# Kernel tuning notes

Hardware: AMD Instinct MI355X
Metric: run time of the kernel (lower is better)

## Reference

```python
import jax, jax.numpy as jnp
import numpy as np

N_NODES = 50000
N_EDGES = 800000
N_FEAT = 64
N_HID = 64
N_CLASSES = 10
N_GRAPHS = 64


def setup_inputs() -> dict:
    key = jax.random.key(0)
    ks = jax.random.split(key, 14)
    # edge_index with no self-loops (PyG add_remaining_self_loops then appends
    # exactly one self loop per node, which the reference reproduces)
    row = jax.random.randint(ks[0], (N_EDGES,), 0, N_NODES, dtype=jnp.int32)
    off = jax.random.randint(ks[1], (N_EDGES,), 1, N_NODES, dtype=jnp.int32)
    col = (row + off) % N_NODES
    edge_index = jnp.stack([row, col])
    batch = jnp.sort(jax.random.randint(ks[2], (N_NODES,), 0, N_GRAPHS, dtype=jnp.int32))
    x = jax.random.normal(ks[3], (N_NODES, N_FEAT), jnp.float32)
    P_vec = jax.random.normal(ks[4], (N_EDGES,), jnp.float32)

    def lin(k, fi, fo):
        return jax.random.normal(k, (fi, fo), jnp.float32) * (1.0 / np.sqrt(fi))

    return {
        "x": x, "edge_index": edge_index, "batch": batch, "P_vec": P_vec,
        "W1": lin(ks[5], N_FEAT, N_HID), "b1": jax.random.normal(ks[6], (N_HID,)) * 0.02,
        "W2": lin(ks[7], N_HID, N_HID), "b2": jax.random.normal(ks[8], (N_HID,)) * 0.02,
        "W3": lin(ks[9], N_HID, N_HID), "b3": jax.random.normal(ks[10], (N_HID,)) * 0.02,
        "Wl": lin(ks[11], N_HID, N_CLASSES), "bl": jax.random.normal(ks[12], (N_CLASSES,)) * 0.02,
    }


def reference(x, edge_index, batch, P_vec, W1, b1, W2, b2, W3, b3, Wl, bl):
    n = x.shape[0]
    row, col = edge_index[0], edge_index[1]
    # add_remaining_self_loops: append one self loop per node with weight 1.0
    sl = jnp.arange(n, dtype=row.dtype)
    fr = jnp.concatenate([row, sl])          # [E+N] source
    fc = jnp.concatenate([col, sl])          # [E+N] target (flow source_to_target)
    w = jnp.concatenate([jax.nn.sigmoid(P_vec), jnp.ones((n,), x.dtype)])
    deg = jax.ops.segment_sum(w, fc, num_segments=n)
    dis = jnp.where(deg > 0, deg ** -0.5, 0.0)  # deg_inv_sqrt, inf->0
    norm = dis[fr] * w * dis[fc]             # identical for all 3 conv layers

    def gcn_layer(h, W, b):
        h = h @ W                             # Linear (no bias inside lin)
        agg = jax.ops.segment_sum(norm[:, None] * h[fr], fc, num_segments=n)
        return agg + b

    h = jax.nn.relu(gcn_layer(x, W1, b1))
    h = jax.nn.relu(gcn_layer(h, W2, b2))
    h = gcn_layer(h, W3, b3)
    # global_mean_pool over batch segment ids
    sums = jax.ops.segment_sum(h, batch, num_segments=N_GRAPHS)
    cnt = jax.ops.segment_sum(jnp.ones((n, 1), h.dtype), batch, num_segments=N_GRAPHS)
    pooled = sums / jnp.maximum(cnt, 1.0)
    # dropout is identity at inference; final classifier
    return pooled @ Wl + bl
```

## Files before the change

### kernel.cpp

```cpp
#include <hip/hip_runtime.h>
#include <hip/hip_bf16.h>
#include <hip/hip_fp16.h>
#include <math.h>

#define N_GRAPHS 64
#define N_CLASSES 10
#define FIXSCALE 262144.0f
#define MAXDEG 64

typedef __hip_bfloat16 bf16;
typedef int          i32x4 __attribute__((ext_vector_type(4)));
typedef _Float16     f16x8 __attribute__((ext_vector_type(8)));
typedef float        f32x4 __attribute__((ext_vector_type(4)));

__device__ __forceinline__ unsigned int pack_edge(int r, float s) {
    return ((unsigned int)r << 16) | (unsigned int)__half_as_ushort(__float2half(s));
}

__global__ void init_k(unsigned int* __restrict__ packed,
                       float* __restrict__ sums, float* __restrict__ cntG, int n) {
    int i = blockIdx.x * 256 + threadIdx.x;
    if (i < n) packed[i] = 0u;
    if (i < N_GRAPHS * 64) sums[i] = 0.0f;
    if (i < N_GRAPHS) cntG[i] = 0.0f;
}

__device__ __forceinline__ int bucket_of(int c) {
    int b = (int)(((unsigned int)c * 41u) >> 18);
    return b > 7 ? 7 : b;
}

__device__ __forceinline__ void do_edge(int c, int e, int myb,
                                        const int* __restrict__ row,
                                        const float* __restrict__ P,
                                        unsigned int* __restrict__ packed,
                                        unsigned int* __restrict__ ell) {
    if (bucket_of(c) == myb) {
        float s = 1.0f / (1.0f + expf(-P[e]));
        unsigned int rec = pack_edge(row[e], s);
        unsigned int fix = (unsigned int)(s * FIXSCALE + 0.5f);
        unsigned int old = atomicAdd(&packed[c], (1u << 24) | fix);
        unsigned int rank = old >> 24;
        if (rank < MAXDEG) ell[c * MAXDEG + rank] = rec;
    }
}

__global__ __launch_bounds__(256) void hist_k(const float* __restrict__ P,
                                              const int* __restrict__ row,
                                              const int* __restrict__ col,
                                              unsigned int* __restrict__ packed,
                                              unsigned int* __restrict__ ell, int E) {
    const int myb = blockIdx.x & 7;
    const int slice = blockIdx.x >> 3;
    const int E4 = E >> 2;
    const i32x4* col4 = (const i32x4*)col;
#pragma unroll
    for (int k = 0; k < 4; ++k) {
        int i4 = slice * 1024 + k * 256 + (int)threadIdx.x;
        if (i4 < E4) {
            i32x4 c = col4[i4];
            int e = i4 * 4;
            do_edge(c[0], e + 0, myb, row, P, packed, ell);
            do_edge(c[1], e + 1, myb, row, P, packed, ell);
            do_edge(c[2], e + 2, myb, row, P, packed, ell);
            do_edge(c[3], e + 3, myb, row, P, packed, ell);
        }
    }
    if (slice == 0) {
        for (int e = E4 * 4 + (int)threadIdx.x; e < E; e += 256)
            do_edge(col[e], e, myb, row, P, packed, ell);
    }
}

__global__ void disxg_k(const unsigned int* __restrict__ packed,
                        const float* __restrict__ x,
                        float* __restrict__ dis, bf16* __restrict__ xg,
                        unsigned int* __restrict__ ell, int n) {
    int i = blockIdx.x * 256 + threadIdx.x;
    if (i < n * 64) {
        int node = i >> 6;
        int lane = i & 63;
        unsigned int pk = packed[node];
        float deg = 1.0f + (float)(pk & 0xFFFFFFu) * (1.0f / FIXSCALE);
        float dv = 1.0f / sqrtf(deg);
        xg[i] = __float2bfloat16(x[i] * dv);
        if (lane == 0) dis[node] = dv;
        int cnt = (int)(pk >> 24);
        if (cnt > MAXDEG) cnt = MAXDEG;
        int pad = ((cnt + 7) & ~7) - cnt;
        if (lane < pad) ell[node * MAXDEG + cnt + lane] = 0u;
    }
}

__global__ void fold_k(const float* __restrict__ W3, const float* __restrict__ b3,
                       const float* __restrict__ Wl, const float* __restrict__ bl,
                       const float* __restrict__ W1, const float* __restrict__ W2,
                       float* __restrict__ Wc, float* __restrict__ bc,
                       __half* __restrict__ W1h, __half* __restrict__ W2h) {
    int t = blockIdx.x * 256 + threadIdx.x;
    if (t < 64 * N_CLASSES) {
        int k = t / N_CLASSES, c = t % N_CLASSES;
        float acc = 0.0f;
        for (int m = 0; m < 64; ++m) acc += W3[k * 64 + m] * Wl[m * N_CLASSES + c];
        Wc[t] = acc;
    }
    if (t < N_CLASSES) {
        float acc = bl[t];
        for (int m = 0; m < 64; ++m) acc += b3[m] * Wl[m * N_CLASSES + t];
        bc[t] = acc;
    }
    if (t < 8192) {
        int u = t & 4095;
        int j = u & 7, lane = (u >> 3) & 63, k2 = (u >> 9) & 1, tt = u >> 10;
        int srow = k2 * 32 + (lane >> 4) * 8 + j;
        int scol = tt * 16 + (lane & 15);
        const float* W = (t < 4096) ? W1 : W2;
        __half* Wh = (t < 4096) ? W1h : W2h;
        Wh[u] = __float2half(W[srow * 64 + scol]);
    }
}

__device__ __forceinline__ float edge_term(unsigned int v, const bf16* g, int lane) {
    int r = (int)(v >> 16);
    float s = __half2float(__ushort_as_half((unsigned short)(v & 0xFFFFu)));
    return s * __bfloat162float(g[r * 64 + lane]);
}

template <int OUTF>
__global__ __launch_bounds__(256) void agg_k(const bf16* __restrict__ g,
                                             const unsigned int* __restrict__ ell,
                                             const unsigned int* __restrict__ packed,
                                             const float* __restrict__ dis,
                                             float* __restrict__ out,
                                             __half* __restrict__ outH, int n) {
    int tid = threadIdx.x;
    int node = __builtin_amdgcn_readfirstlane(blockIdx.x * 4 + (tid >> 6));
    if (node >= n) return;
    int lane = tid & 63;

    float d = dis[node];
    int cnt = (int)(packed[node] >> 24);
    if (cnt > MAXDEG) cnt = MAXDEG;
    int cnt8 = (cnt + 7) & ~7;
    float acc = __bfloat162float(g[node * 64 + lane]);
    const unsigned int* rowp = ell + node * MAXDEG;

    float a[8];
#pragma unroll
    for (int t = 0; t < 8; ++t) a[t] = 0.0f;
    for (int j = 0; j < cnt8; j += 8) {
        unsigned int v[8];
#pragma unroll
        for (int t = 0; t < 8; ++t) v[t] = rowp[j + t];
#pragma unroll
        for (int t = 0; t < 8; ++t) a[t] += edge_term(v[t], g, lane);
    }
#pragma unroll
    for (int off = 4; off >= 1; off >>= 1)
#pragma unroll
        for (int t = 0; t < off; ++t) a[t] += a[t + off];
    acc += a[0];
    acc *= d;

    if (OUTF == 1) outH[(size_t)node * 64 + lane] = __float2half(acc);
    else           out[(size_t)node * 64 + lane] = acc;
}

__global__ __launch_bounds__(256) void gemm_k(const __half* __restrict__ A,
                                              const __half* __restrict__ Wsw,
                                              const float* __restrict__ b,
                                              const float* __restrict__ dis,
                                              bf16* __restrict__ outg, int n) {
    int tid = threadIdx.x;
    int grp = blockIdx.x * 4 + (tid >> 6);
    int rbase = grp * 16;
    if (rbase >= n) return;
    int l = tid & 63, lr = l & 15, lh = l >> 4;

    const f16x8* Ap = (const f16x8*)(A + (size_t)(rbase + lr) * 64 + lh * 8);
    f16x8 a0 = Ap[0];
    f16x8 a1 = Ap[4];
    const f16x8* Wp = (const f16x8*)Wsw;

    float dv[4];
#pragma unroll
    for (int r = 0; r < 4; ++r) dv[r] = dis[rbase + lh * 4 + r];

#pragma unroll
    for (int t = 0; t < 4; ++t) {
        f32x4 acc = {0.0f, 0.0f, 0.0f, 0.0f};
        acc = __builtin_amdgcn_mfma_f32_16x16x32_f16(a0, Wp[(t * 2 + 0) * 64 + l], acc, 0, 0, 0);
        acc = __builtin_amdgcn_mfma_f32_16x16x32_f16(a1, Wp[(t * 2 + 1) * 64 + l], acc, 0, 0, 0);
        int col = t * 16 + lr;
        float bc_ = b[col];
#pragma unroll
        for (int r = 0; r < 4; ++r) {
            float v = fmaxf(acc[r] + bc_, 0.0f) * dv[r];
            outg[(size_t)(rbase + lh * 4 + r) * 64 + col] = __float2bfloat16(v);
        }
    }
}

__global__ __launch_bounds__(256) void poolpart_k(const float* __restrict__ h,
                                                  const int* __restrict__ batch,
                                                  float* __restrict__ sums,
                                                  float* __restrict__ cntG, int n) {
    int wave = threadIdx.x >> 6, lane = threadIdx.x & 63;
    int base = blockIdx.x * 128 + wave * 32;
    if (base >= n) return;
    int end = base + 32; if (end > n) end = n;
    int g = batch[base];
    float acc = 0.0f;
    int run = 0;
    for (int i = base; i < end; ++i) {
        int gi = batch[i];
        if (gi != g) {
            atomicAdd(&sums[g * 64 + lane], acc);
            if (lane == 0) atomicAdd(&cntG[g], (float)run);
            g = gi; acc = 0.0f; run = 0;
        }
        acc += h[i * 64 + lane];
        ++run;
    }
    atomicAdd(&sums[g * 64 + lane], acc);
    if (lane == 0) atomicAdd(&cntG[g], (float)run);
}

__global__ void classify_k(const float* __restrict__ sums, const float* __restrict__ cntG,
                           const float* __restrict__ Wc, const float* __restrict__ bc,
                           float* __restrict__ out) {
    __shared__ float pooled[64];
    int g = blockIdx.x;
    int t = threadIdx.x;
    float inv = 1.0f / fmaxf(cntG[g], 1.0f);
    pooled[t] = sums[g * 64 + t] * inv;
    __syncthreads();
    if (t < N_CLASSES) {
        float acc = bc[t];
        for (int k = 0; k < 64; ++k) acc += pooled[k] * Wc[k * N_CLASSES + t];
        out[g * N_CLASSES + t] = acc;
    }
}

extern "C" void kernel_launch(void* const* d_in, const int* in_sizes, int n_in,
                              void* d_out, int out_size, void* d_ws, size_t ws_size,
                              hipStream_t stream) {
    const float* x     = (const float*)d_in[0];
    const int*   eidx  = (const int*)d_in[1];
    const int*   batch = (const int*)d_in[2];
    const float* P     = (const float*)d_in[3];
    const float* W1 = (const float*)d_in[4];
    const float* b1 = (const float*)d_in[5];
    const float* W2 = (const float*)d_in[6];
    const float* b2 = (const float*)d_in[7];
    const float* W3 = (const float*)d_in[8];
    const float* b3 = (const float*)d_in[9];
    const float* Wl = (const float*)d_in[10];
    const float* bl = (const float*)d_in[11];
    float* out = (float*)d_out;

    const int N = in_sizes[2];
    const int E = in_sizes[3];
    const int* row = eidx;
    const int* col = eidx + E;

    char* p = (char*)d_ws;
    unsigned int* ell = (unsigned int*)p; p += (size_t)N * MAXDEG * 4;
    float* bufF     = (float*)p; p += (size_t)N * 64 * 4;
    bf16*  xg       = (bf16*)p;  p += (size_t)N * 64 * 2;
    bf16*  gA       = (bf16*)p;  p += (size_t)N * 64 * 2;
    __half* aH      = (__half*)p; p += (size_t)N * 64 * 2;
    unsigned int* packed = (unsigned int*)p; p += (size_t)N * 4;
    float* dis      = (float*)p; p += (size_t)N * 4;
    float* sums     = (float*)p; p += (size_t)N_GRAPHS * 64 * 4;
    float* cntG     = (float*)p; p += (size_t)N_GRAPHS * 4;
    float* Wc       = (float*)p; p += (size_t)64 * N_CLASSES * 4;
    __half* W1h     = (__half*)p; p += 4096 * 2;
    __half* W2h     = (__half*)p; p += 4096 * 2;
    float* bc       = (float*)p; p += (size_t)N_CLASSES * 4;
    bf16*  gB       = xg;

    dim3 blk(256);
    int nodeG = (N + 255) / 256;
    int bigG  = (N * 64 + 255) / 256;

    init_k<<<nodeG, blk, 0, stream>>>(packed, sums, cntG, N);
    int nslice = ((E >> 2) + 1023) / 1024;
    hist_k<<<nslice * 8, blk, 0, stream>>>(P, row, col, packed, ell, E);
    disxg_k<<<bigG, blk, 0, stream>>>(packed, x, dis, xg, ell, N);
    fold_k<<<32, blk, 0, stream>>>(W3, b3, Wl, bl, W1, W2, Wc, bc, W1h, W2h);

    int aggG  = (N + 3) / 4;
    int gemmG = (N / 16 + 3) / 4;

    agg_k<1><<<aggG, blk, 0, stream>>>(xg, ell, packed, dis, nullptr, aH, N);
    gemm_k<<<gemmG, blk, 0, stream>>>(aH, W1h, b1, dis, gA, N);
    agg_k<1><<<aggG, blk, 0, stream>>>(gA, ell, packed, dis, nullptr, aH, N);
    gemm_k<<<gemmG, blk, 0, stream>>>(aH, W2h, b2, dis, gB, N);
    agg_k<0><<<aggG, blk, 0, stream>>>(gB, ell, packed, dis, bufF, nullptr, N);

    int poolG = (N + 127) / 128;
    poolpart_k<<<poolG, blk, 0, stream>>>(bufF, batch, sums, cntG, N);
    classify_k<<<N_GRAPHS, dim3(64), 0, stream>>>(sums, cntG, Wc, bc, out);
}
```

Before: 230.2 us.

## Split ELL neighbor lists by source half and aggregate in two passes

Edges are partitioned by whether the source node lies in the lower or upper half. Each half keeps its own counter, and the ELL row is filled from both ends: low sources from the front, high sources from the back. Each aggregation becomes two kernel passes, one gathering only low-half sources and one only high-half sources, so each pass's gather working set is half of g and fits better in cache. In exchange, a float partial buffer must be written and read between passes, there are extra launches, and the histogram kernel now uses vectorised row/P loads with a fixed grid of 2048 blocks.

```diff
diff --git a/kernel.cpp b/kernel.cpp
--- a/kernel.cpp
+++ b/kernel.cpp
@@ -10,6 +10,7 @@
 
 typedef __hip_bfloat16 bf16;
 typedef int          i32x4 __attribute__((ext_vector_type(4)));
+typedef float        f32x4v __attribute__((ext_vector_type(4)));
 typedef _Float16     f16x8 __attribute__((ext_vector_type(8)));
 typedef float        f32x4 __attribute__((ext_vector_type(4)));
 
@@ -17,10 +18,10 @@
     return ((unsigned int)r << 16) | (unsigned int)__half_as_ushort(__float2half(s));
 }
 
-__global__ void init_k(unsigned int* __restrict__ packed,
+__global__ void init_k(unsigned int* __restrict__ packedL, unsigned int* __restrict__ packedH,
                        float* __restrict__ sums, float* __restrict__ cntG, int n) {
     int i = blockIdx.x * 256 + threadIdx.x;
-    if (i < n) packed[i] = 0u;
+    if (i < n) { packedL[i] = 0u; packedH[i] = 0u; }
     if (i < N_GRAPHS * 64) sums[i] = 0.0f;
     if (i < N_GRAPHS) cntG[i] = 0.0f;
 }
@@ -30,49 +31,65 @@
     return b > 7 ? 7 : b;
 }
 
-__device__ __forceinline__ void do_edge(int c, int e, int myb,
-                                        const int* __restrict__ row,
-                                        const float* __restrict__ P,
-                                        unsigned int* __restrict__ packed,
-                                        unsigned int* __restrict__ ell) {
-    if (bucket_of(c) == myb) {
-        float s = 1.0f / (1.0f + expf(-P[e]));
-        unsigned int rec = pack_edge(row[e], s);
-        unsigned int fix = (unsigned int)(s * FIXSCALE + 0.5f);
-        unsigned int old = atomicAdd(&packed[c], (1u << 24) | fix);
-        unsigned int rank = old >> 24;
-        if (rank < MAXDEG) ell[c * MAXDEG + rank] = rec;
-    }
-}
-
 __global__ __launch_bounds__(256) void hist_k(const float* __restrict__ P,
                                               const int* __restrict__ row,
                                               const int* __restrict__ col,
-                                              unsigned int* __restrict__ packed,
-                                              unsigned int* __restrict__ ell, int E) {
+                                              unsigned int* __restrict__ packedL,
+                                              unsigned int* __restrict__ packedH,
+                                              unsigned int* __restrict__ ell,
+                                              int E, int halfN) {
     const int myb = blockIdx.x & 7;
     const int slice = blockIdx.x >> 3;
     const int E4 = E >> 2;
-    const i32x4* col4 = (const i32x4*)col;
+    const i32x4*  col4 = (const i32x4*)col;
+    const i32x4*  row4 = (const i32x4*)row;
+    const f32x4v* P4   = (const f32x4v*)P;
 #pragma unroll
     for (int k = 0; k < 4; ++k) {
         int i4 = slice * 1024 + k * 256 + (int)threadIdx.x;
         if (i4 < E4) {
-            i32x4 c = col4[i4];
-            int e = i4 * 4;
-            do_edge(c[0], e + 0, myb, row, P, packed, ell);
-            do_edge(c[1], e + 1, myb, row, P, packed, ell);
-            do_edge(c[2], e + 2, myb, row, P, packed, ell);
-            do_edge(c[3], e + 3, myb, row, P, packed, ell);
+            i32x4  c = col4[i4];
+            i32x4  r = row4[i4];
+            f32x4v p = P4[i4];
+            bool m[4]; bool low[4]; unsigned int rec[4], val[4]; unsigned int* addr[4];
+#pragma unroll
+            for (int t = 0; t < 4; ++t) {
+                float s = 1.0f / (1.0f + expf(-p[t]));
+                m[t] = (bucket_of(c[t]) == myb);
+                low[t] = (r[t] < halfN);
+                rec[t] = pack_edge(r[t], s);
+                val[t] = (1u << 24) | (unsigned int)(s * FIXSCALE + 0.5f);
+                addr[t] = (low[t] ? packedL : packedH) + c[t];
+            }
+            unsigned int old[4];
+#pragma unroll
+            for (int t = 0; t < 4; ++t) if (m[t]) old[t] = atomicAdd(addr[t], val[t]);
+#pragma unroll
+            for (int t = 0; t < 4; ++t) if (m[t]) {
+                unsigned int rank = old[t] >> 24;
+                unsigned int slot = low[t] ? rank : 63u - rank;
+                if (rank < MAXDEG) ell[c[t] * MAXDEG + slot] = rec[t];
+            }
         }
     }
     if (slice == 0) {
-        for (int e = E4 * 4 + (int)threadIdx.x; e < E; e += 256)
-            do_edge(col[e], e, myb, row, P, packed, ell);
-    }
-}
-
-__global__ void disxg_k(const unsigned int* __restrict__ packed,
+        for (int e = E4 * 4 + (int)threadIdx.x; e < E; e += 256) {
+            int c = col[e];
+            if (bucket_of(c) == myb) {
+                float s = 1.0f / (1.0f + expf(-P[e]));
+                int rr = row[e];
+                bool lo = rr < halfN;
+                unsigned int old = atomicAdd((lo ? packedL : packedH) + c,
+                                             (1u << 24) | (unsigned int)(s * FIXSCALE + 0.5f));
+                unsigned int rank = old >> 24;
+                if (rank < MAXDEG) ell[c * MAXDEG + (lo ? rank : 63u - rank)] = pack_edge(rr, s);
+            }
+        }
+    }
+}
+
+__global__ void disxg_k(const unsigned int* __restrict__ packedL,
+                        const unsigned int* __restrict__ packedH,
                         const float* __restrict__ x,
                         float* __restrict__ dis, bf16* __restrict__ xg,
                         unsigned int* __restrict__ ell, int n) {
@@ -80,15 +97,18 @@
     if (i < n * 64) {
         int node = i >> 6;
         int lane = i & 63;
-        unsigned int pk = packed[node];
-        float deg = 1.0f + (float)(pk & 0xFFFFFFu) * (1.0f / FIXSCALE);
+        unsigned int pkL = packedL[node], pkH = packedH[node];
+        float deg = 1.0f + (float)((pkL & 0xFFFFFFu) + (pkH & 0xFFFFFFu)) * (1.0f / FIXSCALE);
         float dv = 1.0f / sqrtf(deg);
         xg[i] = __float2bfloat16(x[i] * dv);
         if (lane == 0) dis[node] = dv;
-        int cnt = (int)(pk >> 24);
-        if (cnt > MAXDEG) cnt = MAXDEG;
-        int pad = ((cnt + 7) & ~7) - cnt;
-        if (lane < pad) ell[node * MAXDEG + cnt + lane] = 0u;
+        int cntL = (int)(pkL >> 24); if (cntL > MAXDEG) cntL = MAXDEG;
+        int cntH = (int)(pkH >> 24); if (cntH > MAXDEG) cntH = MAXDEG;
+        int padL = ((cntL + 7) & ~7) - cntL;
+        int topStart = 64 - cntH;
+        int padH = topStart & 7;
+        if (lane < padL) ell[node * MAXDEG + cntL + lane] = 0u;
+        if (lane >= 8 && lane < 8 + padH) ell[node * MAXDEG + (topStart - padH) + (lane - 8)] = 0u;
     }
 }
 
@@ -126,11 +146,12 @@
     return s * __bfloat162float(g[r * 64 + lane]);
 }
 
-template <int OUTF>
+template <int PASS, int OUTF>
 __global__ __launch_bounds__(256) void agg_k(const bf16* __restrict__ g,
                                              const unsigned int* __restrict__ ell,
-                                             const unsigned int* __restrict__ packed,
+                                             const unsigned int* __restrict__ packedX,
                                              const float* __restrict__ dis,
+                                             float* __restrict__ partial,
                                              float* __restrict__ out,
                                              __half* __restrict__ outH, int n) {
     int tid = threadIdx.x;
@@ -138,17 +159,24 @@
     if (node >= n) return;
     int lane = tid & 63;
 
-    float d = dis[node];
-    int cnt = (int)(packed[node] >> 24);
+    int cnt = (int)(packedX[node] >> 24);
     if (cnt > MAXDEG) cnt = MAXDEG;
-    int cnt8 = (cnt + 7) & ~7;
-    float acc = __bfloat162float(g[node * 64 + lane]);
+    int j0, j1;
+    float acc;
+    if (PASS == 0) {
+        acc = __bfloat162float(g[node * 64 + lane]);
+        j0 = 0; j1 = (cnt + 7) & ~7;
+    } else {
+        acc = partial[(size_t)node * 64 + lane];
+        int topStart = 64 - cnt;
+        j0 = topStart & ~7; j1 = 64;
+    }
     const unsigned int* rowp = ell + node * MAXDEG;
 
     float a[8];
 #pragma unroll
     for (int t = 0; t < 8; ++t) a[t] = 0.0f;
-    for (int j = 0; j < cnt8; j += 8) {
+    for (int j = j0; j < j1; j += 8) {
         unsigned int v[8];
 #pragma unroll
         for (int t = 0; t < 8; ++t) v[t] = rowp[j + t];
@@ -160,10 +188,14 @@
 #pragma unroll
         for (int t = 0; t < off; ++t) a[t] += a[t + off];
     acc += a[0];
-    acc *= d;
-
-    if (OUTF == 1) outH[(size_t)node * 64 + lane] = __float2half(acc);
-    else           out[(size_t)node * 64 + lane] = acc;
+
+    if (PASS == 0) {
+        partial[(size_t)node * 64 + lane] = acc;
+    } else {
+        acc *= dis[node];
+        if (OUTF == 1) outH[(size_t)node * 64 + lane] = __float2half(acc);
+        else           out[(size_t)node * 64 + lane] = acc;
+    }
 }
 
 __global__ __launch_bounds__(256) void gemm_k(const __half* __restrict__ A,
@@ -263,6 +295,7 @@
     const int E = in_sizes[3];
     const int* row = eidx;
     const int* col = eidx + E;
+    const int halfN = N >> 1;
 
     char* p = (char*)d_ws;
     unsigned int* ell = (unsigned int*)p; p += (size_t)N * MAXDEG * 4;
@@ -270,7 +303,8 @@
     bf16*  xg       = (bf16*)p;  p += (size_t)N * 64 * 2;
     bf16*  gA       = (bf16*)p;  p += (size_t)N * 64 * 2;
     __half* aH      = (__half*)p; p += (size_t)N * 64 * 2;
-    unsigned int* packed = (unsigned int*)p; p += (size_t)N * 4;
+    unsigned int* packedL = (unsigned int*)p; p += (size_t)N * 4;
+    unsigned int* packedH = (unsigned int*)p; p += (size_t)N * 4;
     float* dis      = (float*)p; p += (size_t)N * 4;
     float* sums     = (float*)p; p += (size_t)N_GRAPHS * 64 * 4;
     float* cntG     = (float*)p; p += (size_t)N_GRAPHS * 4;
@@ -284,20 +318,22 @@
     int nodeG = (N + 255) / 256;
     int bigG  = (N * 64 + 255) / 256;
 
-    init_k<<<nodeG, blk, 0, stream>>>(packed, sums, cntG, N);
-    int nslice = ((E >> 2) + 1023) / 1024;
-    hist_k<<<nslice * 8, blk, 0, stream>>>(P, row, col, packed, ell, E);
-    disxg_k<<<bigG, blk, 0, stream>>>(packed, x, dis, xg, ell, N);
+    init_k<<<nodeG, blk, 0, stream>>>(packedL, packedH, sums, cntG, N);
+    hist_k<<<2048, blk, 0, stream>>>(P, row, col, packedL, packedH, ell, E, halfN);
+    disxg_k<<<bigG, blk, 0, stream>>>(packedL, packedH, x, dis, xg, ell, N);
     fold_k<<<32, blk, 0, stream>>>(W3, b3, Wl, bl, W1, W2, Wc, bc, W1h, W2h);
 
     int aggG  = (N + 3) / 4;
     int gemmG = (N / 16 + 3) / 4;
 
-    agg_k<1><<<aggG, blk, 0, stream>>>(xg, ell, packed, dis, nullptr, aH, N);
+    agg_k<0, 0><<<aggG, blk, 0, stream>>>(xg, ell, packedL, dis, bufF, nullptr, nullptr, N);
+    agg_k<1, 1><<<aggG, blk, 0, stream>>>(xg, ell, packedH, dis, bufF, nullptr, aH, N);
     gemm_k<<<gemmG, blk, 0, stream>>>(aH, W1h, b1, dis, gA, N);
-    agg_k<1><<<aggG, blk, 0, stream>>>(gA, ell, packed, dis, nullptr, aH, N);
+    agg_k<0, 0><<<aggG, blk, 0, stream>>>(gA, ell, packedL, dis, bufF, nullptr, nullptr, N);
+    agg_k<1, 1><<<aggG, blk, 0, stream>>>(gA, ell, packedH, dis, bufF, nullptr, aH, N);
     gemm_k<<<gemmG, blk, 0, stream>>>(aH, W2h, b2, dis, gB, N);
-    agg_k<0><<<aggG, blk, 0, stream>>>(gB, ell, packed, dis, bufF, nullptr, N);
+    agg_k<0, 0><<<aggG, blk, 0, stream>>>(gB, ell, packedL, dis, bufF, nullptr, nullptr, N);
+    agg_k<1, 0><<<aggG, blk, 0, stream>>>(gB, ell, packedH, dis, bufF, bufF, nullptr, N);
 
     int poolG = (N + 127) / 128;
     poolpart_k<<<poolG, blk, 0, stream>>>(bufF, batch, sums, cntG, N);
```

Measured after the change: 263.1 us. 14.3% more time.
